# Performance work log

Measured on AMD Instinct MI355X. Metric: run time of the kernel, lower is better.

Reference implementation:

```python
import math
import jax, jax.numpy as jnp
import numpy as np

B, T, C = 4, 2048, 1024
H = 16
D = C // H  # head dim = 64


def setup_inputs() -> dict:
    key = jax.random.key(0)
    ks = jax.random.split(key, 9)
    s = 0.02
    return {
        "x": jax.random.normal(ks[0], (B, T, C), dtype=jnp.float32),
        "Wq": jax.random.normal(ks[1], (C, C), dtype=jnp.float32) * s,
        "bq": jax.random.normal(ks[2], (C,), dtype=jnp.float32) * s,
        "Wk": jax.random.normal(ks[3], (C, C), dtype=jnp.float32) * s,
        "bk": jax.random.normal(ks[4], (C,), dtype=jnp.float32) * s,
        "Wv": jax.random.normal(ks[5], (C, C), dtype=jnp.float32) * s,
        "bv": jax.random.normal(ks[6], (C,), dtype=jnp.float32) * s,
        "Wo": jax.random.normal(ks[7], (C, C), dtype=jnp.float32) * s,
        "bo": jax.random.normal(ks[8], (C,), dtype=jnp.float32) * s,
    }


def reference(x, Wq, bq, Wk, bk, Wv, bv, Wo, bo):
    # Linear projections (torch Linear: x @ W.T + b), split into heads -> [B,H,T,D]
    def heads(y):
        return y.reshape(B, T, H, D).transpose(0, 2, 1, 3)

    q = heads(x @ Wq.T + bq)
    k = heads(x @ Wk.T + bk)
    v = heads(x @ Wv.T + bv)

    # Full [B,H,T,T] score matrix, scaled by 1/sqrt(D) (no mask, dropout=0 / eval)
    scores = jnp.einsum("bhqd,bhkd->bhqk", q, k) / math.sqrt(D)
    attn = jax.nn.softmax(scores, axis=-1)
    out = jnp.einsum("bhqk,bhkd->bhqd", attn, v)
    out = out.transpose(0, 2, 1, 3).reshape(B, T, C)
    return out @ Wo.T + bo
```

## Files before the change

### kernel.cpp

```cpp
#include <hip/hip_runtime.h>
#include <hip/hip_bf16.h>
#include <stdint.h>

#define Bb 4
#define Tt 2048
#define Cc 1024
#define Hh 16
#define Dd 64

using bf16x8 = __bf16 __attribute__((ext_vector_type(8)));
using f32x4  = float  __attribute__((ext_vector_type(4)));
using f32x2  = float  __attribute__((ext_vector_type(2)));
using f32x16 = float  __attribute__((ext_vector_type(16)));
typedef unsigned short u16;
typedef unsigned int   u32;

#if defined(__has_builtin) && __has_builtin(__builtin_amdgcn_exp2f)
#define EXP2F(x) __builtin_amdgcn_exp2f(x)
#else
#define EXP2F(x) exp2f(x)
#endif

#if defined(__has_builtin) && __has_builtin(__builtin_amdgcn_permlane32_swap)
#define PERMLANE32_SWAP(a, b)                                          \
  do {                                                                 \
    auto _r = __builtin_amdgcn_permlane32_swap((a), (b), false, false);\
    (a) = _r[0]; (b) = _r[1];                                          \
  } while (0)
#else
#define PERMLANE32_SWAP(a, b) \
  asm volatile("v_permlane32_swap_b32 %0, %1" : "+v"(a), "+v"(b))
#endif

__device__ __forceinline__ unsigned cvt_pk_bf16(float lo, float hi) {
  unsigned r;
  asm("v_cvt_pk_bf16_f32 %0, %1, %2" : "=v"(r) : "v"(lo), "v"(hi));
  return r;
}

__device__ __forceinline__ u16 f32_to_bf16(float f) {
  union { float f; unsigned u; } v; v.f = f;
  unsigned r = v.u + 0x7fffu + ((v.u >> 16) & 1u);
  return (u16)(r >> 16);
}

__device__ __forceinline__ void gl2lds16(const u16* g, u16* l) {
  __builtin_amdgcn_global_load_lds(
      (const __attribute__((address_space(1))) u32*)g,
      (__attribute__((address_space(3))) u32*)l, 16, 0, 0);
}

__global__ void cast_f32_to_bf16(const float* __restrict__ in, u16* __restrict__ out, int n) {
  int i = (blockIdx.x * blockDim.x + threadIdx.x) * 4;
  if (i >= n) return;
  float4 v = *reinterpret_cast<const float4*>(in + i);
  ushort4 o;
  o.x = f32_to_bf16(v.x); o.y = f32_to_bf16(v.y);
  o.z = f32_to_bf16(v.z); o.w = f32_to_bf16(v.w);
  *reinterpret_cast<ushort4*>(out + i) = o;
}

__global__ void cast4_f32_to_bf16(const float* __restrict__ w0, const float* __restrict__ w1,
                                  const float* __restrict__ w2, const float* __restrict__ w3,
                                  u16* __restrict__ o0, u16* __restrict__ o1,
                                  u16* __restrict__ o2, u16* __restrict__ o3, int n) {
  const float* in; u16* out;
  switch (blockIdx.y) {
    case 0: in = w0; out = o0; break;
    case 1: in = w1; out = o1; break;
    case 2: in = w2; out = o2; break;
    default: in = w3; out = o3; break;
  }
  int i = (blockIdx.x * blockDim.x + threadIdx.x) * 4;
  if (i >= n) return;
  float4 v = *reinterpret_cast<const float4*>(in + i);
  ushort4 o;
  o.x = f32_to_bf16(v.x); o.y = f32_to_bf16(v.y);
  o.z = f32_to_bf16(v.z); o.w = f32_to_bf16(v.w);
  *reinterpret_cast<ushort4*>(out + i) = o;
}

__global__ __launch_bounds__(256, 3)
void gemm_qkv(const u16* __restrict__ A, const u16* __restrict__ Bqkv,
              const float* __restrict__ bq, const float* __restrict__ bk,
              const float* __restrict__ bv,
              u16* __restrict__ qout, u16* __restrict__ kout, u16* __restrict__ vtout,
              float qscl)
{
  constexpr int K = Cc, BK = 64, LDT = 136;
  __shared__ alignas(16) u16 smem[128 * LDT];
  u16* As = smem;
  u16* Bs = smem + 128 * 64;
  const int tid  = threadIdx.x;
  const int wave = tid >> 6, lane = tid & 63;
  const int lid = blockIdx.x;
  const int xcd = lid & 7, cch = lid >> 3;
  const int bx = xcd * 8 + (cch & 7), by = cch >> 3;
  const int row0 = bx * 128, col0 = by * 128;
  const int seg  = col0 >> 10;
  const int wm = (wave & 1) * 64, wn = (wave >> 1) * 64;
  const int fr = lane & 15, qd = lane >> 4;
  const int srow = lane >> 3;
  const int scol = ((lane & 7) ^ srow) << 3;

  f32x4 acc[4][4] = {};
  const u16* pA = A    + (size_t)(row0 + wave * 32 + srow) * K + scol;
  const u16* pB = Bqkv + (size_t)(col0 + wave * 32 + srow) * K + scol;

  for (int k0 = 0; k0 < K; k0 += BK) {
#pragma unroll
    for (int c = 0; c < 4; ++c) {
      gl2lds16(pA + (size_t)(c * 8) * K + k0, &As[(wave * 32 + c * 8) * 64]);
      gl2lds16(pB + (size_t)(c * 8) * K + k0, &Bs[(wave * 32 + c * 8) * 64]);
    }
    __syncthreads();
#pragma unroll
    for (int kk = 0; kk < 2; ++kk) {
      bf16x8 af[4], bf[4];
#pragma unroll
      for (int i = 0; i < 4; ++i) {
        int ra = wm + i * 16 + fr;
        af[i] = *reinterpret_cast<const bf16x8*>(
            &As[ra * 64 + (((kk * 4 + qd) ^ (ra & 7)) << 3)]);
        int rb = wn + i * 16 + fr;
        bf[i] = *reinterpret_cast<const bf16x8*>(
            &Bs[rb * 64 + (((kk * 4 + qd) ^ (rb & 7)) << 3)]);
      }
#pragma unroll
      for (int i = 0; i < 4; ++i)
#pragma unroll
        for (int j = 0; j < 4; ++j)
          acc[i][j] = __builtin_amdgcn_mfma_f32_16x16x32_bf16(af[i], bf[j], acc[i][j], 0, 0, 0);
    }
    __syncthreads();
  }

  const float* bias = (seg == 0) ? bq : ((seg == 1) ? bk : bv);
  const float scale = (seg == 0) ? qscl : 1.0f;
  const int colL0 = col0 & 1023;

  if (seg < 2) {
    u16* outp = (seg == 0) ? qout : kout;
#pragma unroll
    for (int j = 0; j < 4; ++j) {
      int col = colL0 + wn + j * 16 + fr;
      float bvv = bias[col];
#pragma unroll
      for (int i = 0; i < 4; ++i) {
        int rowb = row0 + wm + i * 16 + (lane >> 4) * 4;
#pragma unroll
        for (int r = 0; r < 4; ++r)
          outp[(size_t)(rowb + r) * Cc + col] = f32_to_bf16((acc[i][j][r] + bvv) * scale);
      }
    }
  } else {
    __syncthreads();
#pragma unroll
    for (int j = 0; j < 4; ++j) {
      int lc = wn + j * 16 + fr;
      float bvv = bias[colL0 + lc];
#pragma unroll
      for (int i = 0; i < 4; ++i) {
        int lr = wm + i * 16 + (lane >> 4) * 4;
#pragma unroll
        for (int r = 0; r < 4; ++r)
          smem[lc * LDT + lr + r] = f32_to_bf16(acc[i][j][r] + bvv);
      }
    }
    __syncthreads();
    int lc = tid >> 1, seg2 = tid & 1;
    int col = colL0 + lc;
    int h = col >> 6, d = col & 63;
    int bb = row0 >> 11, t0 = (row0 & 2047) + seg2 * 64;
    u16* dst = vtout + ((size_t)(bb * Hh + h) * Dd + d) * Tt + t0;
    const u16* src = &smem[lc * LDT + seg2 * 64];
#pragma unroll
    for (int g = 0; g < 8; ++g)
      *reinterpret_cast<uint4*>(dst + g * 8) = *reinterpret_cast<const uint4*>(src + g * 8);
  }
}

__global__ __launch_bounds__(256, 3)
void gemm_out(const u16* __restrict__ A, const u16* __restrict__ Bw,
              const float* __restrict__ bias, float* __restrict__ Cout,
              int M, int N, int K)
{
  constexpr int BK = 64;
  __shared__ alignas(16) u16 As[128 * 64];
  __shared__ alignas(16) u16 Bs[128 * 64];
  const int tid  = threadIdx.x;
  const int wave = tid >> 6, lane = tid & 63;
  const int lid = blockIdx.x;
  const int xcd = lid & 7, cch = lid >> 3;
  const int bx = xcd * 8 + (cch & 7), by = cch >> 3;
  const int row0 = bx * 128, col0 = by * 128;
  const int wm = (wave & 1) * 64, wn = (wave >> 1) * 64;
  const int fr = lane & 15, qd = lane >> 4;
  const int srow = lane >> 3;
  const int scol = ((lane & 7) ^ srow) << 3;

  f32x4 acc[4][4] = {};
  const u16* pA = A  + (size_t)(row0 + wave * 32 + srow) * K + scol;
  const u16* pB = Bw + (size_t)(col0 + wave * 32 + srow) * K + scol;

  for (int k0 = 0; k0 < K; k0 += BK) {
#pragma unroll
    for (int c = 0; c < 4; ++c) {
      gl2lds16(pA + (size_t)(c * 8) * K + k0, &As[(wave * 32 + c * 8) * 64]);
      gl2lds16(pB + (size_t)(c * 8) * K + k0, &Bs[(wave * 32 + c * 8) * 64]);
    }
    __syncthreads();
#pragma unroll
    for (int kk = 0; kk < 2; ++kk) {
      bf16x8 af[4], bf[4];
#pragma unroll
      for (int i = 0; i < 4; ++i) {
        int ra = wm + i * 16 + fr;
        af[i] = *reinterpret_cast<const bf16x8*>(
            &As[ra * 64 + (((kk * 4 + qd) ^ (ra & 7)) << 3)]);
        int rb = wn + i * 16 + fr;
        bf[i] = *reinterpret_cast<const bf16x8*>(
            &Bs[rb * 64 + (((kk * 4 + qd) ^ (rb & 7)) << 3)]);
      }
#pragma unroll
      for (int i = 0; i < 4; ++i)
#pragma unroll
        for (int j = 0; j < 4; ++j)
          acc[i][j] = __builtin_amdgcn_mfma_f32_16x16x32_bf16(af[i], bf[j], acc[i][j], 0, 0, 0);
    }
    __syncthreads();
  }

#pragma unroll
  for (int j = 0; j < 4; ++j) {
    int col = col0 + wn + j * 16 + fr;
    float bv = bias[col];
#pragma unroll
    for (int i = 0; i < 4; ++i) {
      int rowb = row0 + wm + i * 16 + (lane >> 4) * 4;
#pragma unroll
      for (int r = 0; r < 4; ++r)
        Cout[(size_t)(rowb + r) * N + col] = acc[i][j][r] + bv;
    }
  }
}

__global__ __launch_bounds__(256, 4)
void attn_kernel(const u16* __restrict__ Q, const u16* __restrict__ Kmat,
                 const u16* __restrict__ VT, u16* __restrict__ O) {
  __shared__ alignas(16) unsigned char smem[32768];
  float* OfT = (float*)smem;
  float* Qs  = (float*)(smem + 17408);

  const int tid = threadIdx.x, wave = tid >> 6, lane = tid & 63;
  const int l31 = lane & 31, hi = lane >> 5;
  const int qt = wave >> 1, kh = wave & 1;
  const int bh = blockIdx.x, qt0 = blockIdx.y;
  const int b = bh >> 4, h = bh & 15;
  const size_t base = (size_t)b * Tt * Cc + (size_t)h * Dd;
  const size_t vtb = (size_t)bh * Dd * Tt;

  bf16x8 qb[4];
  {
    const u16* qp = Q + base + (size_t)(qt0 * 64 + qt * 32 + l31) * Cc + hi * 8;
#pragma unroll
    for (int c = 0; c < 4; ++c)
      qb[c] = *reinterpret_cast<const bf16x8*>(qp + c * 16);
  }

  f32x16 Oacc[2] = {};
  f32x2 sacc = {0.f, 0.f};

  const u16* pK = Kmat + base + (size_t)(wave * 16 + (lane >> 3)) * Cc +
                  (((lane & 7) ^ (lane >> 3)) << 3);
  const u16* pV = VT + vtb + (size_t)(wave * 16 + (lane >> 3)) * Tt +
                  (((lane & 7) ^ (lane >> 3)) << 3);

  auto STAGE = [&](int buf, int kt) {
    u16* Kd = (u16*)(smem + (buf << 14)) + wave * 1024;
    u16* Vd = Kd + 4096;
    const u16* pk = pK + (size_t)kt * Cc;
    const u16* pv = pV + kt;
#pragma unroll
    for (int c = 0; c < 2; ++c) {
      gl2lds16(pk + (size_t)(c * 8) * Cc, Kd + c * 512);
      gl2lds16(pv + (size_t)(c * 8) * Tt, Vd + c * 512);
    }
  };

  STAGE(0, 0);
  __syncthreads();

  int cur = 0;
#pragma unroll 1
  for (int t = 0; t < 32; ++t) {
    if (t < 31) STAGE(cur ^ 1, (t + 1) << 6);

    const u16* Ks = (const u16*)(smem + (cur << 14));
    const u16* Vs = Ks + 4096;

    bf16x8 ka[4], vb[2][2];
    const int key = kh * 32 + l31;
#pragma unroll
    for (int c = 0; c < 4; ++c)
      ka[c] = *reinterpret_cast<const bf16x8*>(
          &Ks[key * 64 + ((((c << 1) + hi) ^ (key & 7)) << 3)]);
#pragma unroll
    for (int k0i = 0; k0i < 2; ++k0i)
#pragma unroll
      for (int dh = 0; dh < 2; ++dh) {
        int drow = dh * 32 + l31;
        int ch = kh * 4 + k0i * 2 + hi;
        vb[k0i][dh] = *reinterpret_cast<const bf16x8*>(
            &Vs[drow * 64 + ((ch ^ (drow & 7)) << 3)]);
      }

    __builtin_amdgcn_s_setprio(1);

    f32x16 s = {};
#pragma unroll
    for (int c = 0; c < 4; ++c)
      s = __builtin_amdgcn_mfma_f32_32x32x16_bf16(ka[c], qb[c], s, 0, 0, 0);
    unsigned pk8[8];
#pragma unroll
    for (int i = 0; i < 8; ++i) {
      float p0 = EXP2F(s[2 * i]), p1 = EXP2F(s[2 * i + 1]);
      sacc += (f32x2){p0, p1};
      pk8[i] = cvt_pk_bf16(p0, p1);
    }
    unsigned a0 = pk8[0], a1 = pk8[1], a2 = pk8[2], a3 = pk8[3];
    unsigned b0 = pk8[4], b1 = pk8[5], b2 = pk8[6], b3 = pk8[7];
    PERMLANE32_SWAP(a0, a2);
    PERMLANE32_SWAP(a1, a3);
    PERMLANE32_SWAP(b0, b2);
    PERMLANE32_SWAP(b1, b3);
    union { unsigned u[4]; bf16x8 v; } plo, phi;
    plo.u[0] = a0; plo.u[1] = a1; plo.u[2] = a2; plo.u[3] = a3;
    phi.u[0] = b0; phi.u[1] = b1; phi.u[2] = b2; phi.u[3] = b3;
    Oacc[0] = __builtin_amdgcn_mfma_f32_32x32x16_bf16(plo.v, vb[0][0], Oacc[0], 0, 0, 0);
    Oacc[1] = __builtin_amdgcn_mfma_f32_32x32x16_bf16(plo.v, vb[0][1], Oacc[1], 0, 0, 0);
    Oacc[0] = __builtin_amdgcn_mfma_f32_32x32x16_bf16(phi.v, vb[1][0], Oacc[0], 0, 0, 0);
    Oacc[1] = __builtin_amdgcn_mfma_f32_32x32x16_bf16(phi.v, vb[1][1], Oacc[1], 0, 0, 0);

    __builtin_amdgcn_s_setprio(0);

    __syncthreads();
    cur ^= 1;
  }

  {
    float s = sacc[0] + sacc[1];
    s += __shfl_xor(s, 32, 64);
    if (hi == 0) Qs[wave * 32 + l31] = s;
  }

#pragma unroll
  for (int step = 0; step < 2; ++step) {
    if (kh == step) {
#pragma unroll
      for (int dh = 0; dh < 2; ++dh) {
        int d = dh * 32 + l31;
        float* rowp = &OfT[d * 68 + qt * 32 + hi * 4];
#pragma unroll
        for (int g = 0; g < 4; ++g) {
          f32x4 v;
          v[0] = Oacc[dh][g * 4 + 0]; v[1] = Oacc[dh][g * 4 + 1];
          v[2] = Oacc[dh][g * 4 + 2]; v[3] = Oacc[dh][g * 4 + 3];
          float* dst = rowp + g * 8;
          if (step == 0) *reinterpret_cast<f32x4*>(dst) = v;
          else {
            f32x4 old = *reinterpret_cast<const f32x4*>(dst);
            *reinterpret_cast<f32x4*>(dst) = old + v;
          }
        }
      }
    }
    __syncthreads();
  }

  {
    int q = tid >> 2, dg = tid & 3;
    float qtot = Qs[(q >> 5) * 64 + (q & 31)] + Qs[(q >> 5) * 64 + 32 + (q & 31)];
    float linv = 1.0f / qtot;
    alignas(16) u16 tmp[16];
#pragma unroll
    for (int i = 0; i < 16; ++i)
      tmp[i] = f32_to_bf16(OfT[(dg * 16 + i) * 68 + q] * linv);
    u16* op = O + base + (size_t)(qt0 * 64 + q) * Cc + dg * 16;
    *reinterpret_cast<uint4*>(op)     = *reinterpret_cast<const uint4*>(tmp);
    *reinterpret_cast<uint4*>(op + 8) = *reinterpret_cast<const uint4*>(tmp + 8);
  }
}

extern "C" void kernel_launch(void* const* d_in, const int* in_sizes, int n_in,
                              void* d_out, int out_size, void* d_ws, size_t ws_size,
                              hipStream_t stream) {
  const float* x  = (const float*)d_in[0];
  const float* Wq = (const float*)d_in[1];
  const float* bq = (const float*)d_in[2];
  const float* Wk = (const float*)d_in[3];
  const float* bk = (const float*)d_in[4];
  const float* Wv = (const float*)d_in[5];
  const float* bv = (const float*)d_in[6];
  const float* Wo = (const float*)d_in[7];
  const float* bo = (const float*)d_in[8];

  const size_t NX = (size_t)Bb * Tt * Cc;
  const size_t NW = (size_t)Cc * Cc;

  u16* ws  = (u16*)d_ws;
  u16* xb  = ws;
  u16* wqb = ws + NX;
  u16* wkb = wqb + NW;
  u16* wvb = wkb + NW;
  u16* wob = wvb + NW;
  u16* qb  = wob + NW;
  u16* kb  = qb + NX;
  u16* vtb = kb + NX;
  u16* attnb = xb;

  cast_f32_to_bf16<<<(int)(NX / 4 / 256), 256, 0, stream>>>(x, xb, (int)NX);
  cast4_f32_to_bf16<<<dim3((unsigned)(NW / 4 / 256), 4), 256, 0, stream>>>(
      Wq, Wk, Wv, Wo, wqb, wkb, wvb, wob, (int)NW);

  const float QSCL = 0.125f * 1.44269504f;
  gemm_qkv<<<dim3(1536), 256, 0, stream>>>(xb, wqb, bq, bk, bv, qb, kb, vtb, QSCL);

  attn_kernel<<<dim3(Bb * Hh, Tt / 64), 256, 0, stream>>>(qb, kb, vtb, attnb);

  gemm_out<<<dim3(512), 256, 0, stream>>>(attnb, wob, bo, (float*)d_out,
                                          Bb * Tt, Cc, Cc);
}
```

Measured before the change: 270.6 us.

## Double-buffer GEMM k-tiles with BK=32 and split attention launch in halves

```diff
diff --git a/kernel.cpp b/kernel.cpp
--- a/kernel.cpp
+++ b/kernel.cpp
@@ -87,10 +87,8 @@
               u16* __restrict__ qout, u16* __restrict__ kout, u16* __restrict__ vtout,
               float qscl)
 {
-  constexpr int K = Cc, BK = 64, LDT = 136;
+  constexpr int K = Cc, LDT = 136;
   __shared__ alignas(16) u16 smem[128 * LDT];
-  u16* As = smem;
-  u16* Bs = smem + 128 * 64;
   const int tid  = threadIdx.x;
   const int wave = tid >> 6, lane = tid & 63;
   const int lid = blockIdx.x;
@@ -100,39 +98,47 @@
   const int seg  = col0 >> 10;
   const int wm = (wave & 1) * 64, wn = (wave >> 1) * 64;
   const int fr = lane & 15, qd = lane >> 4;
-  const int srow = lane >> 3;
-  const int scol = ((lane & 7) ^ srow) << 3;
+  const int soff = (((lane & 3) ^ ((lane >> 2) & 3)) << 3);
+  const u16* pA = A    + (size_t)(row0 + wave * 32 + (lane >> 2)) * K + soff;
+  const u16* pB = Bqkv + (size_t)(col0 + wave * 32 + (lane >> 2)) * K + soff;
 
   f32x4 acc[4][4] = {};
-  const u16* pA = A    + (size_t)(row0 + wave * 32 + srow) * K + scol;
-  const u16* pB = Bqkv + (size_t)(col0 + wave * 32 + srow) * K + scol;
-
-  for (int k0 = 0; k0 < K; k0 += BK) {
-#pragma unroll
-    for (int c = 0; c < 4; ++c) {
-      gl2lds16(pA + (size_t)(c * 8) * K + k0, &As[(wave * 32 + c * 8) * 64]);
-      gl2lds16(pB + (size_t)(c * 8) * K + k0, &Bs[(wave * 32 + c * 8) * 64]);
-    }
+
+  auto STAGE = [&](int buf, int k0) {
+    u16* Ad = smem + buf * 8192 + wave * 1024;
+    u16* Bd = smem + buf * 8192 + 4096 + wave * 1024;
+    gl2lds16(pA + k0,            Ad);
+    gl2lds16(pA + (size_t)16 * K + k0, Ad + 512);
+    gl2lds16(pB + k0,            Bd);
+    gl2lds16(pB + (size_t)16 * K + k0, Bd + 512);
+  };
+
+  STAGE(0, 0);
+  __syncthreads();
+
+  int cur = 0;
+#pragma unroll 1
+  for (int t = 0; t < 32; ++t) {
+    if (t < 31) STAGE(cur ^ 1, (t + 1) * 32);
+    const u16* As = smem + cur * 8192;
+    const u16* Bs = As + 4096;
+    bf16x8 af[4], bf[4];
+#pragma unroll
+    for (int i = 0; i < 4; ++i) {
+      int ra = wm + i * 16 + fr;
+      af[i] = *reinterpret_cast<const bf16x8*>(&As[ra * 32 + ((qd ^ (ra & 3)) << 3)]);
+      int rb = wn + i * 16 + fr;
+      bf[i] = *reinterpret_cast<const bf16x8*>(&Bs[rb * 32 + ((qd ^ (rb & 3)) << 3)]);
+    }
+    __builtin_amdgcn_s_setprio(1);
+#pragma unroll
+    for (int i = 0; i < 4; ++i)
+#pragma unroll
+      for (int j = 0; j < 4; ++j)
+        acc[i][j] = __builtin_amdgcn_mfma_f32_16x16x32_bf16(af[i], bf[j], acc[i][j], 0, 0, 0);
+    __builtin_amdgcn_s_setprio(0);
     __syncthreads();
-#pragma unroll
-    for (int kk = 0; kk < 2; ++kk) {
-      bf16x8 af[4], bf[4];
-#pragma unroll
-      for (int i = 0; i < 4; ++i) {
-        int ra = wm + i * 16 + fr;
-        af[i] = *reinterpret_cast<const bf16x8*>(
-            &As[ra * 64 + (((kk * 4 + qd) ^ (ra & 7)) << 3)]);
-        int rb = wn + i * 16 + fr;
-        bf[i] = *reinterpret_cast<const bf16x8*>(
-            &Bs[rb * 64 + (((kk * 4 + qd) ^ (rb & 7)) << 3)]);
-      }
-#pragma unroll
-      for (int i = 0; i < 4; ++i)
-#pragma unroll
-        for (int j = 0; j < 4; ++j)
-          acc[i][j] = __builtin_amdgcn_mfma_f32_16x16x32_bf16(af[i], bf[j], acc[i][j], 0, 0, 0);
-    }
-    __syncthreads();
+    cur ^= 1;
   }
 
   const float* bias = (seg == 0) ? bq : ((seg == 1) ? bk : bv);
@@ -154,7 +160,6 @@
       }
     }
   } else {
-    __syncthreads();
 #pragma unroll
     for (int j = 0; j < 4; ++j) {
       int lc = wn + j * 16 + fr;
@@ -185,9 +190,7 @@
               const float* __restrict__ bias, float* __restrict__ Cout,
               int M, int N, int K)
 {
-  constexpr int BK = 64;
-  __shared__ alignas(16) u16 As[128 * 64];
-  __shared__ alignas(16) u16 Bs[128 * 64];
+  __shared__ alignas(16) u16 smem[16384];
   const int tid  = threadIdx.x;
   const int wave = tid >> 6, lane = tid & 63;
   const int lid = blockIdx.x;
@@ -196,39 +199,47 @@
   const int row0 = bx * 128, col0 = by * 128;
   const int wm = (wave & 1) * 64, wn = (wave >> 1) * 64;
   const int fr = lane & 15, qd = lane >> 4;
-  const int srow = lane >> 3;
-  const int scol = ((lane & 7) ^ srow) << 3;
+  const int soff = (((lane & 3) ^ ((lane >> 2) & 3)) << 3);
+  const u16* pA = A  + (size_t)(row0 + wave * 32 + (lane >> 2)) * K + soff;
+  const u16* pB = Bw + (size_t)(col0 + wave * 32 + (lane >> 2)) * K + soff;
 
   f32x4 acc[4][4] = {};
-  const u16* pA = A  + (size_t)(row0 + wave * 32 + srow) * K + scol;
-  const u16* pB = Bw + (size_t)(col0 + wave * 32 + srow) * K + scol;
-
-  for (int k0 = 0; k0 < K; k0 += BK) {
-#pragma unroll
-    for (int c = 0; c < 4; ++c) {
-      gl2lds16(pA + (size_t)(c * 8) * K + k0, &As[(wave * 32 + c * 8) * 64]);
-      gl2lds16(pB + (size_t)(c * 8) * K + k0, &Bs[(wave * 32 + c * 8) * 64]);
-    }
+
+  auto STAGE = [&](int buf, int k0) {
+    u16* Ad = smem + buf * 8192 + wave * 1024;
+    u16* Bd = smem + buf * 8192 + 4096 + wave * 1024;
+    gl2lds16(pA + k0,            Ad);
+    gl2lds16(pA + (size_t)16 * K + k0, Ad + 512);
+    gl2lds16(pB + k0,            Bd);
+    gl2lds16(pB + (size_t)16 * K + k0, Bd + 512);
+  };
+
+  STAGE(0, 0);
+  __syncthreads();
+
+  int cur = 0;
+#pragma unroll 1
+  for (int t = 0; t < 32; ++t) {
+    if (t < 31) STAGE(cur ^ 1, (t + 1) * 32);
+    const u16* As = smem + cur * 8192;
+    const u16* Bs = As + 4096;
+    bf16x8 af[4], bf[4];
+#pragma unroll
+    for (int i = 0; i < 4; ++i) {
+      int ra = wm + i * 16 + fr;
+      af[i] = *reinterpret_cast<const bf16x8*>(&As[ra * 32 + ((qd ^ (ra & 3)) << 3)]);
+      int rb = wn + i * 16 + fr;
+      bf[i] = *reinterpret_cast<const bf16x8*>(&Bs[rb * 32 + ((qd ^ (rb & 3)) << 3)]);
+    }
+    __builtin_amdgcn_s_setprio(1);
+#pragma unroll
+    for (int i = 0; i < 4; ++i)
+#pragma unroll
+      for (int j = 0; j < 4; ++j)
+        acc[i][j] = __builtin_amdgcn_mfma_f32_16x16x32_bf16(af[i], bf[j], acc[i][j], 0, 0, 0);
+    __builtin_amdgcn_s_setprio(0);
     __syncthreads();
-#pragma unroll
-    for (int kk = 0; kk < 2; ++kk) {
-      bf16x8 af[4], bf[4];
-#pragma unroll
-      for (int i = 0; i < 4; ++i) {
-        int ra = wm + i * 16 + fr;
-        af[i] = *reinterpret_cast<const bf16x8*>(
-            &As[ra * 64 + (((kk * 4 + qd) ^ (ra & 7)) << 3)]);
-        int rb = wn + i * 16 + fr;
-        bf[i] = *reinterpret_cast<const bf16x8*>(
-            &Bs[rb * 64 + (((kk * 4 + qd) ^ (rb & 7)) << 3)]);
-      }
-#pragma unroll
-      for (int i = 0; i < 4; ++i)
-#pragma unroll
-        for (int j = 0; j < 4; ++j)
-          acc[i][j] = __builtin_amdgcn_mfma_f32_16x16x32_bf16(af[i], bf[j], acc[i][j], 0, 0, 0);
-    }
-    __syncthreads();
+    cur ^= 1;
   }
 
 #pragma unroll
@@ -247,7 +258,7 @@
 
 __global__ __launch_bounds__(256, 4)
 void attn_kernel(const u16* __restrict__ Q, const u16* __restrict__ Kmat,
-                 const u16* __restrict__ VT, u16* __restrict__ O) {
+                 const u16* __restrict__ VT, u16* __restrict__ O, int qt0_base) {
   __shared__ alignas(16) unsigned char smem[32768];
   float* OfT = (float*)smem;
   float* Qs  = (float*)(smem + 17408);
@@ -255,7 +266,7 @@
   const int tid = threadIdx.x, wave = tid >> 6, lane = tid & 63;
   const int l31 = lane & 31, hi = lane >> 5;
   const int qt = wave >> 1, kh = wave & 1;
-  const int bh = blockIdx.x, qt0 = blockIdx.y;
+  const int bh = blockIdx.x, qt0 = qt0_base + blockIdx.y;
   const int b = bh >> 4, h = bh & 15;
   const size_t base = (size_t)b * Tt * Cc + (size_t)h * Dd;
   const size_t vtb = (size_t)bh * Dd * Tt;
@@ -426,7 +437,8 @@
   const float QSCL = 0.125f * 1.44269504f;
   gemm_qkv<<<dim3(1536), 256, 0, stream>>>(xb, wqb, bq, bk, bv, qb, kb, vtb, QSCL);
 
-  attn_kernel<<<dim3(Bb * Hh, Tt / 64), 256, 0, stream>>>(qb, kb, vtb, attnb);
+  attn_kernel<<<dim3(Bb * Hh, 16), 256, 0, stream>>>(qb, kb, vtb, attnb, 0);
+  attn_kernel<<<dim3(Bb * Hh, 16), 256, 0, stream>>>(qb, kb, vtb, attnb, 16);
 
   gemm_out<<<dim3(512), 256, 0, stream>>>(attnb, wob, bo, (float*)d_out,
                                           Bb * Tt, Cc, Cc);
```

New measurement: 284.7 us. 5.2% more time.
